# Kernel tuning notes

Hardware: AMD Instinct MI355X
Metric: run time of the kernel (lower is better)

The kernel has to match this reference:

```python
import jax, jax.numpy as jnp
import numpy as np

# PyTorch GRU cell math (gate order: r, z, n)

def _gru_cell(x, h, Wih_l, Whh_l, bih_l, bhh_l):
    # x: [B,F], h: [B,F]
    xg = x @ Wih_l.T + bih_l          # [B,3F]
    hg = h @ Whh_l.T + bhh_l          # [B,3F]
    xr, xz, xn = jnp.split(xg, 3, axis=-1)
    hr, hz, hn = jnp.split(hg, 3, axis=-1)
    r = jax.nn.sigmoid(xr + hr)
    z = jax.nn.sigmoid(xz + hz)
    n = jnp.tanh(xn + r * hn)
    return (1.0 - z) * n + z * h


def _gru_seq(x, Wih_l, Whh_l, bih_l, bhh_l):
    # x: [B,S,Fin] -> (outputs [B,S,F], last hidden [B,F]); zero initial state
    B, S, _ = x.shape
    F = Whh_l.shape[1]
    xg = jnp.einsum('bsi,gi->bsg', x, Wih_l) + bih_l  # [B,S,3F]
    def step(h, xg_t):
        hg = h @ Whh_l.T + bhh_l
        xr, xz, xn = jnp.split(xg_t, 3, axis=-1)
        hr, hz, hn = jnp.split(hg, 3, axis=-1)
        r = jax.nn.sigmoid(xr + hr)
        z = jax.nn.sigmoid(xz + hz)
        n = jnp.tanh(xn + r * hn)
        h_new = (1.0 - z) * n + z * h
        return h_new, h_new
    h0 = jnp.zeros((B, F), dtype=x.dtype)
    hT, ys = jax.lax.scan(step, h0, jnp.swapaxes(xg, 0, 1))
    return jnp.swapaxes(ys, 0, 1), hT


def setup_inputs() -> dict:
    key = jax.random.key(0)
    B, H, T = 32, 48, 16
    S_DIM, A_DIM, R_DIM, F, L = 64, 16, 8, 256, 2
    ks = jax.random.split(key, 20)
    k = 1.0 / np.sqrt(F)
    def xav(kk, shape):
        fan_in, fan_out = shape[1], shape[0]
        lim = np.sqrt(6.0 / (fan_in + fan_out))
        return jax.random.uniform(kk, shape, jnp.float32, -lim, lim)
    return {
        'history_s': jax.random.normal(ks[0], (B, H, S_DIM), jnp.float32),
        'history_a': jax.random.normal(ks[1], (B, H, A_DIM), jnp.float32),
        'present_s': jax.random.normal(ks[2], (B, S_DIM), jnp.float32),
        'future_a':  jax.random.normal(ks[3], (B, T, A_DIM), jnp.float32),
        'Ws':  xav(ks[4], (F, S_DIM)),
        'bs':  jnp.zeros((F,), jnp.float32),
        'Wa':  xav(ks[5], (F, A_DIM)),
        'ba':  jnp.zeros((F,), jnp.float32),
        'Wih': jax.random.uniform(ks[6], (L, 3 * F, F), jnp.float32, -k, k),
        'Whh': jax.random.uniform(ks[7], (L, 3 * F, F), jnp.float32, -k, k),
        'bih': jax.random.uniform(ks[8], (L, 3 * F), jnp.float32, -k, k),
        'bhh': jax.random.uniform(ks[9], (L, 3 * F), jnp.float32, -k, k),
        'Wr':  xav(ks[10], (R_DIM, F)),
        'br':  jnp.zeros((R_DIM,), jnp.float32),
        'Wso': xav(ks[11], (S_DIM, F)),
        'bso': jnp.zeros((S_DIM,), jnp.float32),
    }


def reference(history_s, history_a, present_s, future_a,
              Ws, bs, Wa, ba, Wih, Whh, bih, bhh, Wr, br, Wso, bso):
    # drop_rate = 0 -> DeterministicDropout is identity. Since the GRU is causal,
    # and the history prefix (history_s_a) is unchanged across rollout iterations,
    # re-running the GRU over the full growing history each step (the original
    # O(T^2) loop) is mathematically identical to carrying hidden state
    # incrementally. We implement the exact-equivalent O(T) form.
    L = Wih.shape[0]
    B = present_s.shape[0]
    F = Whh.shape[2]

    # embed history and run the stacked GRU over it once (zero init state)
    hist = jnp.einsum('bhs,fs->bhf', history_s, Ws) + bs \
         + jnp.einsum('bha,fa->bhf', history_a, Wa) + ba
    seq = jnp.tanh(hist)                                   # [B,H,F]
    hiddens = []
    for l in range(L):
        seq, hT = _gru_seq(seq, Wih[l], Whh[l], bih[l], bhh[l])
        hiddens.append(hT)
    hidden0 = jnp.stack(hiddens, axis=0)                   # [L,B,F]

    present_feat = present_s @ Ws.T + bs                   # [B,F]
    fa_feat = jnp.einsum('bta,fa->btf', future_a, Wa) + ba # [B,T,F]

    def rollout(carry, fa_t):
        pf, hidden = carry
        x = jnp.tanh(pf + fa_t)                            # [B,F]
        new_h = []
        inp = x
        for l in range(L):
            h_l = _gru_cell(inp, hidden[l], Wih[l], Whh[l], bih[l], bhh[l])
            new_h.append(h_l)
            inp = h_l
        hidden_new = jnp.stack(new_h, axis=0)
        r = jnp.tanh(inp @ Wr.T + br)                      # [B,R]
        s = jnp.tanh(inp @ Wso.T + bso)                    # [B,S]
        pf_new = s @ Ws.T + bs
        return (pf_new, hidden_new), (r, s)

    (_, _), (rs, ss) = jax.lax.scan(rollout, (present_feat, hidden0),
                                    jnp.swapaxes(fa_feat, 0, 1))
    future_r = jnp.swapaxes(rs, 0, 1)                      # [B,T,R]
    future_s = jnp.swapaxes(ss, 0, 1)                      # [B,T,S]
    return future_r, future_s
```

## Files before the change

### kernel.cpp

```cpp
#include <hip/hip_runtime.h>
#include <math.h>


#define BLK 256
#define CH  36
#define BST 292

#define O_XQ    0
#define O_HQ    1168
#define O_H1Q   2336
#define O_PART  3504
#define O_SST   6768
#define O_BI    7024
#define O_BH    7072
#define O_BSO   7120
#define O_BR    7184
#define O_WSOF  7200
#define O_WRF   23840
#define LDS_FLOATS 25920
#define LDS_BYTES  (LDS_FLOATS * 4)

#define O_SEQ  0
#define O_H0R  393216
#define O_H1R  917504
#define WS_FLOATS 1441792
#define POISON_BYTES (WS_FLOATS * 4)

using vf4 = __attribute__((ext_vector_type(4))) float;

__device__ __forceinline__ float dotv(vf4 a, vf4 b, float acc) {
  acc = fmaf(a[0], b[0], acc); acc = fmaf(a[1], b[1], acc);
  acc = fmaf(a[2], b[2], acc); acc = fmaf(a[3], b[3], acc);
  return acc;
}
__device__ __forceinline__ float hsum(vf4 v) { return (v[0]+v[1]) + (v[2]+v[3]); }

__device__ __forceinline__ bool valid4(vf4 v) {
  return fabsf(v[0]) < 1.0e30f && fabsf(v[1]) < 1.0e30f &&
         fabsf(v[2]) < 1.0e30f && fabsf(v[3]) < 1.0e30f;
}

__device__ __forceinline__ void llc_issue4(vf4& v, const float* p) {
  asm volatile("global_load_dwordx4 %0, %1, off sc0 sc1"
               : "=&v"(v) : "v"(p) : "memory");
}
__device__ __forceinline__ void llc_storef(float* p, float v) {
  asm volatile("global_store_dword %0, %1, off sc0 sc1" :: "v"(p), "v"(v) : "memory");
}
__device__ __forceinline__ void vwait() {
  asm volatile("s_waitcnt vmcnt(0)" ::: "memory");
  __builtin_amdgcn_sched_barrier(0);
}

extern "C" __global__ void __launch_bounds__(BLK, 1)
gru_rollout_kernel(const float* __restrict__ hist_s,
                   const float* __restrict__ hist_a,
                   const float* __restrict__ present_s,
                   const float* __restrict__ future_a,
                   const float* __restrict__ Ws, const float* __restrict__ bs,
                   const float* __restrict__ Wa, const float* __restrict__ ba,
                   const float* __restrict__ Wih, const float* __restrict__ Whh,
                   const float* __restrict__ bih, const float* __restrict__ bhh,
                   const float* __restrict__ Wr, const float* __restrict__ br,
                   const float* __restrict__ Wso, const float* __restrict__ bso,
                   float* __restrict__ out, float* __restrict__ wsf)
{
  extern __shared__ float lds[];
  float* XQ   = lds + O_XQ;
  float* HQ   = lds + O_HQ;
  float* H1Q  = lds + O_H1Q;
  float* PART = lds + O_PART;
  float* SST  = lds + O_SST;
  float* BI   = lds + O_BI;
  float* BH   = lds + O_BH;
  float* BSO  = lds + O_BSO;
  float* BR   = lds + O_BR;
  float* WSOF = lds + O_WSOF;
  float* WRF  = lds + O_WRF;

  const int tid = threadIdx.x;
  const int bid = blockIdx.x;
  const int gid = bid & 7;
  const int mem = bid >> 3;
  const bool isL0 = (mem < 16);
  const int fc = mem & 15;
  const int layer = isL0 ? 0 : 1;

  const int jp = tid >> 4;
  const int ks = tid & 15;

  float* seq = wsf + O_SEQ;
  float* h0r = wsf + O_H0R;
  float* h1r = wsf + O_H1R;

  const int sb = tid >> 6, srem = tid & 63;
  const int sko = srem >> 3, ssl = srem & 7;
  const int goff = sko * 32 + ssl * 4;
  const int loff = sb * BST + sko * CH + ssl * 4;
  const int gvec = (gid * 4 + sb) * 256 + goff;

  auto poll1 = [&](float* d, const float* p) {
    vf4 v; int g = 0;
    for (;;) {
      llc_issue4(v, p); vwait();
      if (valid4(v) || ++g > (1 << 18)) break;
    }
    *(vf4*)d = v;
  };
  auto poll2 = [&](float* d1, const float* p1, float* d2, const float* p2) {
    vf4 v1, v2; int g = 0;
    for (;;) {
      llc_issue4(v1, p1); llc_issue4(v2, p2); vwait();
      if ((valid4(v1) && valid4(v2)) || ++g > (1 << 18)) break;
    }
    *(vf4*)d1 = v1; *(vf4*)d2 = v2;
  };
  auto zeroH = [&](float* d) { *(vf4*)d = (vf4){0.f, 0.f, 0.f, 0.f}; };

  vf4 w[3][8];
  {
    const float* src = (ks < 8) ? Wih : Whh;
    const int cb = (ks & 7) * 32;
    #pragma unroll
    for (int r = 0; r < 3; ++r) {
      int j = jp * 3 + r;
      int grow = (layer * 768) + (j >> 4) * 256 + fc * 16 + (j & 15);
      const float* wr = src + grow * 256 + cb;
      #pragma unroll
      for (int c = 0; c < 8; ++c) w[r][c] = *(const vf4*)(wr + c * 4);
    }
  }
  const float* xq_base = (ks < 8) ? (XQ + ks * CH) : (HQ + (ks - 8) * CH);

  auto cell = [&](float* dst) {
    __syncthreads();
    float a0[4], a1[4], a2[4];
    #pragma unroll
    for (int b = 0; b < 4; ++b) { a0[b] = 0.f; a1[b] = 0.f; a2[b] = 0.f; }
    #pragma unroll
    for (int b = 0; b < 4; ++b) {
      const vf4* xb = (const vf4*)(xq_base + b * BST);
      vf4 x0 = xb[0], x1 = xb[1], x2 = xb[2], x3 = xb[3];
      vf4 x4 = xb[4], x5 = xb[5], x6 = xb[6], x7 = xb[7];
      float a = a0[b];
      a = dotv(w[0][0], x0, a); a = dotv(w[0][1], x1, a);
      a = dotv(w[0][2], x2, a); a = dotv(w[0][3], x3, a);
      a = dotv(w[0][4], x4, a); a = dotv(w[0][5], x5, a);
      a = dotv(w[0][6], x6, a); a = dotv(w[0][7], x7, a);
      a0[b] = a; a = a1[b];
      a = dotv(w[1][0], x0, a); a = dotv(w[1][1], x1, a);
      a = dotv(w[1][2], x2, a); a = dotv(w[1][3], x3, a);
      a = dotv(w[1][4], x4, a); a = dotv(w[1][5], x5, a);
      a = dotv(w[1][6], x6, a); a = dotv(w[1][7], x7, a);
      a1[b] = a; a = a2[b];
      a = dotv(w[2][0], x0, a); a = dotv(w[2][1], x1, a);
      a = dotv(w[2][2], x2, a); a = dotv(w[2][3], x3, a);
      a = dotv(w[2][4], x4, a); a = dotv(w[2][5], x5, a);
      a = dotv(w[2][6], x6, a); a = dotv(w[2][7], x7, a);
      a2[b] = a;
    }
    #pragma unroll
    for (int b = 0; b < 4; ++b) {
      PART[(jp * 3 + 0) * 68 + b * 16 + ks] = a0[b];
      PART[(jp * 3 + 1) * 68 + b * 16 + ks] = a1[b];
      PART[(jp * 3 + 2) * 68 + b * 16 + ks] = a2[b];
    }
    __syncthreads();
    if (tid < 64) {
      int i = tid >> 2, b = tid & 3;
      const vf4* pr4 = (const vf4*)(PART + i * 68 + b * 16);
      const vf4* pz4 = (const vf4*)(PART + (16 + i) * 68 + b * 16);
      const vf4* pn4 = (const vf4*)(PART + (32 + i) * 68 + b * 16);
      float pr = hsum(pr4[0]) + hsum(pr4[1]) + hsum(pr4[2]) + hsum(pr4[3])
               + BI[i] + BH[i];
      float pz = hsum(pz4[0]) + hsum(pz4[1]) + hsum(pz4[2]) + hsum(pz4[3])
               + BI[16 + i] + BH[16 + i];
      float xn = hsum(pn4[0]) + hsum(pn4[1]) + BI[32 + i];
      float hn = hsum(pn4[2]) + hsum(pn4[3]) + BH[32 + i];
      float rg = 1.f / (1.f + expf(-pr));
      float zg = 1.f / (1.f + expf(-pz));
      float ng = tanhf(xn + rg * hn);
      int f = fc * 16 + i;
      float hp = HQ[b * BST + (f >> 5) * CH + (f & 31)];
      llc_storef(dst + (gid * 4 + b) * 256 + f, (1.f - zg) * ng + zg * hp);
    }
  };

  auto heads = [&](int tt) {
    int so = tid >> 2, b = tid & 3;
    const vf4* wrow = (const vf4*)(WSOF + so * 260);
    float a = BSO[so];
    #pragma unroll
    for (int ko = 0; ko < 8; ++ko) {
      const vf4* hv = (const vf4*)(H1Q + b * BST + ko * CH);
      a = dotv(wrow[ko * 8 + 0], hv[0], a); a = dotv(wrow[ko * 8 + 1], hv[1], a);
      a = dotv(wrow[ko * 8 + 2], hv[2], a); a = dotv(wrow[ko * 8 + 3], hv[3], a);
      a = dotv(wrow[ko * 8 + 4], hv[4], a); a = dotv(wrow[ko * 8 + 5], hv[5], a);
      a = dotv(wrow[ko * 8 + 6], hv[6], a); a = dotv(wrow[ko * 8 + 7], hv[7], a);
    }
    float sv = tanhf(a);
    SST[b * 64 + so] = sv;
    if (mem == 0) {
      out[4096 + ((gid * 4 + b) * 16 + tt) * 64 + so] = sv;
      if (tid < 32) {
        int q = tid >> 2;
        const vf4* wr2 = (const vf4*)(WRF + q * 260);
        float ar = BR[q];
        #pragma unroll
        for (int ko = 0; ko < 8; ++ko) {
          const vf4* hv = (const vf4*)(H1Q + b * BST + ko * CH);
          #pragma unroll
          for (int c = 0; c < 8; ++c) ar = dotv(wr2[ko * 8 + c], hv[c], ar);
        }
        out[((gid * 4 + b) * 16 + tt) * 8 + q] = tanhf(ar);
      }
    }
  };

  auto xdot = [&](int t) {
    const int f = tid;
    float a0 = bs[f], a1 = a0, a2 = a0, a3 = a0;
    const vf4* wsr = (const vf4*)(Ws + f * 64);
    #pragma unroll 4
    for (int c = 0; c < 16; ++c) {
      vf4 wv = wsr[c];
      a0 = dotv(wv, *(const vf4*)(SST + 0 * 64 + c * 4), a0);
      a1 = dotv(wv, *(const vf4*)(SST + 1 * 64 + c * 4), a1);
      a2 = dotv(wv, *(const vf4*)(SST + 2 * 64 + c * 4), a2);
      a3 = dotv(wv, *(const vf4*)(SST + 3 * 64 + c * 4), a3);
    }
    const vf4* war = (const vf4*)(Wa + f * 16);
    vf4 w0 = war[0], w1 = war[1], w2 = war[2], w3 = war[3];
    float x4[4] = {a0, a1, a2, a3};
    #pragma unroll
    for (int b = 0; b < 4; ++b) {
      const vf4* fa = (const vf4*)(future_a + ((gid * 4 + b) * 16 + t) * 16);
      float a = ba[f] + x4[b];
      a = dotv(w0, fa[0], a); a = dotv(w1, fa[1], a);
      a = dotv(w2, fa[2], a); a = dotv(w3, fa[3], a);
      XQ[b * BST + (f >> 5) * CH + (f & 31)] = tanhf(a);
    }
  };

  if (tid < 48) {
    int g = tid >> 4, i = tid & 15;
    int grow = layer * 768 + g * 256 + fc * 16 + i;
    BI[tid] = bih[grow];
    BH[tid] = bhh[grow];
  }
  if (isL0) {
    for (int idx = tid; idx < 64 * 256; idx += BLK) {
      int r = idx >> 8, k = idx & 255;
      WSOF[r * 260 + k] = Wso[r * 256 + k];
    }
    for (int idx = tid; idx < 8 * 256; idx += BLK) {
      int r = idx >> 8, k = idx & 255;
      WRF[r * 260 + k] = Wr[r * 256 + k];
    }
    if (tid < 64) BSO[tid] = bso[tid];
    if (tid < 8)  BR[tid] = br[tid];
  }
  for (int e = mem * 1536 + tid; e < mem * 1536 + 1536; e += BLK) {
    int b = e / 12288, rem = e % 12288, t = rem >> 8, f = rem & 255;
    int gb = gid * 4 + b;
    const float* hs = hist_s + (gb * 48 + t) * 64;
    const float* ha = hist_a + (gb * 48 + t) * 16;
    const float* wsr = Ws + f * 64;
    const float* war = Wa + f * 16;
    float a = bs[f] + ba[f];
    for (int k = 0; k < 64; ++k) a = fmaf(wsr[k], hs[k], a);
    for (int k = 0; k < 16; ++k) a = fmaf(war[k], ha[k], a);
    llc_storef(&seq[(gb * 48 + t) * 256 + f], tanhf(a));
  }
  __syncthreads();

  for (int u = 0; u < 64; ++u) {
    if (isL0) {
      if (u < 48) {
        if (u == 0) {
          poll1(XQ + loff, seq + ((gid * 4 + sb) * 48 + u) * 256 + goff);
          zeroH(HQ + loff);
        } else {
          poll2(XQ + loff, seq + ((gid * 4 + sb) * 48 + u) * 256 + goff,
                HQ + loff, h0r + (u - 1) * 8192 + gvec);
        }
        cell(h0r + u * 8192);
      } else {
        const int t = u - 48;
        if (t == 0) {
          SST[tid] = present_s[(gid * 4 + (tid >> 6)) * 64 + (tid & 63)];
          poll1(HQ + loff, h0r + (u - 1) * 8192 + gvec);
          __syncthreads();
        } else {
          poll2(HQ + loff, h0r + (u - 1) * 8192 + gvec,
                H1Q + loff, h1r + (u - 1) * 8192 + gvec);
          __syncthreads();
          heads(t - 1);
          __syncthreads();
        }
        xdot(t);
        cell(h0r + u * 8192);
      }
    } else {
      if (u == 0) {
        poll1(XQ + loff, h0r + u * 8192 + gvec);
        zeroH(HQ + loff);
      } else {
        poll2(XQ + loff, h0r + u * 8192 + gvec,
              HQ + loff, h1r + (u - 1) * 8192 + gvec);
      }
      cell(h1r + u * 8192);
    }
  }

  if (isL0 && mem == 0) {
    poll1(H1Q + loff, h1r + 63 * 8192 + gvec);
    __syncthreads();
    heads(15);
  }
}

extern "C" void kernel_launch(void* const* d_in, const int* in_sizes, int n_in,
                              void* d_out, int out_size, void* d_ws, size_t ws_size,
                              hipStream_t stream) {
  (void)in_sizes; (void)n_in; (void)out_size; (void)ws_size;
  const float* hist_s    = (const float*)d_in[0];
  const float* hist_a    = (const float*)d_in[1];
  const float* present_s = (const float*)d_in[2];
  const float* future_a  = (const float*)d_in[3];
  const float* Ws  = (const float*)d_in[4];
  const float* bs  = (const float*)d_in[5];
  const float* Wa  = (const float*)d_in[6];
  const float* ba  = (const float*)d_in[7];
  const float* Wih = (const float*)d_in[8];
  const float* Whh = (const float*)d_in[9];
  const float* bih = (const float*)d_in[10];
  const float* bhh = (const float*)d_in[11];
  const float* Wr  = (const float*)d_in[12];
  const float* br  = (const float*)d_in[13];
  const float* Wso = (const float*)d_in[14];
  const float* bso = (const float*)d_in[15];
  float* out = (float*)d_out;
  float* wsf = (float*)d_ws;

  hipMemsetAsync(d_ws, 0x7F, POISON_BYTES, stream);
  hipFuncSetAttribute(reinterpret_cast<const void*>(gru_rollout_kernel),
                      hipFuncAttributeMaxDynamicSharedMemorySize, LDS_BYTES);
  hipLaunchKernelGGL(gru_rollout_kernel, dim3(256), dim3(BLK), LDS_BYTES, stream,
                     hist_s, hist_a, present_s, future_a,
                     Ws, bs, Wa, ba, Wih, Whh, bih, bhh, Wr, br, Wso, bso,
                     out, wsf);
}
```

Measured before the change: 344.8 us.

## Poll per-slice ready flags instead of poisoned data vectors between GRU steps

Each block now publishes a small per-step, per-layer ready flag after its hidden-state slice is written (wait on stores, then one flag store). Consumers spin on one or two flag words, with s_sleep between attempts, and then read the data in a single burst. Before, they repeatedly reloaded full data vectors and checked them for poison values. This is meant to cut LLC traffic and contention from many blocks spinning on wide loads. In exchange, every recurrent step gets an extra store-wait and an extra flag-then-data round trip on the critical path.

```diff
diff --git a/kernel.cpp b/kernel.cpp
--- a/kernel.cpp
+++ b/kernel.cpp
@@ -23,7 +23,8 @@
 #define O_SEQ  0
 #define O_H0R  393216
 #define O_H1R  917504
-#define WS_FLOATS 1441792
+#define O_CAN  1441792
+#define WS_FLOATS 1458176
 #define POISON_BYTES (WS_FLOATS * 4)
 
 using vf4 = __attribute__((ext_vector_type(4))) float;
@@ -43,6 +44,19 @@
 __device__ __forceinline__ void llc_issue4(vf4& v, const float* p) {
   asm volatile("global_load_dwordx4 %0, %1, off sc0 sc1"
                : "=&v"(v) : "v"(p) : "memory");
+}
+__device__ __forceinline__ float llc_loadf(const float* p) {
+  float v;
+  asm volatile("global_load_dword %0, %1, off sc0 sc1\n\ts_waitcnt vmcnt(0)"
+               : "=&v"(v) : "v"(p) : "memory");
+  return v;
+}
+__device__ __forceinline__ void llc_loadf2(float& a, float& b,
+                                           const float* p0, const float* p1) {
+  asm volatile("global_load_dword %0, %2, off sc0 sc1\n\t"
+               "global_load_dword %1, %3, off sc0 sc1\n\t"
+               "s_waitcnt vmcnt(0)"
+               : "=&v"(a), "=&v"(b) : "v"(p0), "v"(p1) : "memory");
 }
 __device__ __forceinline__ void llc_storef(float* p, float v) {
   asm volatile("global_store_dword %0, %1, off sc0 sc1" :: "v"(p), "v"(v) : "memory");
@@ -92,28 +106,53 @@
   float* seq = wsf + O_SEQ;
   float* h0r = wsf + O_H0R;
   float* h1r = wsf + O_H1R;
+  float* can = wsf + O_CAN;
 
   const int sb = tid >> 6, srem = tid & 63;
   const int sko = srem >> 3, ssl = srem & 7;
   const int goff = sko * 32 + ssl * 4;
   const int loff = sb * BST + sko * CH + ssl * 4;
   const int gvec = (gid * 4 + sb) * 256 + goff;
-
-  auto poll1 = [&](float* d, const float* p) {
+  const int slice = goff >> 4;
+
+  auto canp = [&](int u, int l) {
+    return can + ((u * 8 + gid) * 2 + l) * 16 + slice;
+  };
+  auto canp_mine = [&](int u) {
+    return can + ((u * 8 + gid) * 2 + layer) * 16 + fc;
+  };
+
+  auto cpoll1 = [&](const float* c) {
+    int g = 0;
+    while (llc_loadf(c) > 2.0f) {
+      __builtin_amdgcn_s_sleep(1);
+      if (++g > (1 << 18)) break;
+    }
+  };
+  auto cpoll2 = [&](const float* c0, const float* c1) {
+    int g = 0;
+    for (;;) {
+      float a, b;
+      llc_loadf2(a, b, c0, c1);
+      if ((a < 2.0f && b < 2.0f) || ++g > (1 << 18)) break;
+      __builtin_amdgcn_s_sleep(1);
+    }
+  };
+  auto burst1 = [&](float* d, const float* p) {
+    vf4 v; llc_issue4(v, p); vwait(); *(vf4*)d = v;
+  };
+  auto burst2 = [&](float* d1, const float* p1, float* d2, const float* p2) {
+    vf4 v1, v2; llc_issue4(v1, p1); llc_issue4(v2, p2); vwait();
+    *(vf4*)d1 = v1; *(vf4*)d2 = v2;
+  };
+  auto dpoll1 = [&](float* d, const float* p) {
     vf4 v; int g = 0;
     for (;;) {
       llc_issue4(v, p); vwait();
       if (valid4(v) || ++g > (1 << 18)) break;
+      __builtin_amdgcn_s_sleep(1);
     }
     *(vf4*)d = v;
-  };
-  auto poll2 = [&](float* d1, const float* p1, float* d2, const float* p2) {
-    vf4 v1, v2; int g = 0;
-    for (;;) {
-      llc_issue4(v1, p1); llc_issue4(v2, p2); vwait();
-      if ((valid4(v1) && valid4(v2)) || ++g > (1 << 18)) break;
-    }
-    *(vf4*)d1 = v1; *(vf4*)d2 = v2;
   };
   auto zeroH = [&](float* d) { *(vf4*)d = (vf4){0.f, 0.f, 0.f, 0.f}; };
 
@@ -132,7 +171,7 @@
   }
   const float* xq_base = (ks < 8) ? (XQ + ks * CH) : (HQ + (ks - 8) * CH);
 
-  auto cell = [&](float* dst) {
+  auto cell = [&](float* dst, float* cp) {
     __syncthreads();
     float a0[4], a1[4], a2[4];
     #pragma unroll
@@ -183,6 +222,8 @@
       int f = fc * 16 + i;
       float hp = HQ[b * BST + (f >> 5) * CH + (f & 31)];
       llc_storef(dst + (gid * 4 + b) * 256 + f, (1.f - zg) * ng + zg * hp);
+      asm volatile("s_waitcnt vmcnt(0)" ::: "memory");
+      if (tid == 0) llc_storef(cp, 1.0f);
     }
   };
 
@@ -277,44 +318,60 @@
   for (int u = 0; u < 64; ++u) {
     if (isL0) {
       if (u < 48) {
+        const float* seqp = seq + ((gid * 4 + sb) * 48 + u) * 256 + goff;
         if (u == 0) {
-          poll1(XQ + loff, seq + ((gid * 4 + sb) * 48 + u) * 256 + goff);
+          dpoll1(XQ + loff, seqp);
           zeroH(HQ + loff);
         } else {
-          poll2(XQ + loff, seq + ((gid * 4 + sb) * 48 + u) * 256 + goff,
-                HQ + loff, h0r + (u - 1) * 8192 + gvec);
+          cpoll1(canp(u - 1, 0));
+          vf4 vx, vh;
+          llc_issue4(vx, seqp);
+          llc_issue4(vh, h0r + (u - 1) * 8192 + gvec);
+          vwait();
+          int g = 0;
+          while (!valid4(vx) && ++g < (1 << 18)) {
+            __builtin_amdgcn_s_sleep(1);
+            llc_issue4(vx, seqp); vwait();
+          }
+          *(vf4*)(XQ + loff) = vx;
+          *(vf4*)(HQ + loff) = vh;
         }
-        cell(h0r + u * 8192);
+        cell(h0r + u * 8192, canp_mine(u));
       } else {
         const int t = u - 48;
         if (t == 0) {
           SST[tid] = present_s[(gid * 4 + (tid >> 6)) * 64 + (tid & 63)];
-          poll1(HQ + loff, h0r + (u - 1) * 8192 + gvec);
+          cpoll1(canp(u - 1, 0));
+          burst1(HQ + loff, h0r + (u - 1) * 8192 + gvec);
           __syncthreads();
         } else {
-          poll2(HQ + loff, h0r + (u - 1) * 8192 + gvec,
-                H1Q + loff, h1r + (u - 1) * 8192 + gvec);
+          cpoll2(canp(u - 1, 0), canp(u - 1, 1));
+          burst2(HQ + loff,  h0r + (u - 1) * 8192 + gvec,
+                 H1Q + loff, h1r + (u - 1) * 8192 + gvec);
           __syncthreads();
           heads(t - 1);
           __syncthreads();
         }
         xdot(t);
-        cell(h0r + u * 8192);
+        cell(h0r + u * 8192, canp_mine(u));
       }
     } else {
       if (u == 0) {
-        poll1(XQ + loff, h0r + u * 8192 + gvec);
+        cpoll1(canp(0, 0));
+        burst1(XQ + loff, h0r + gvec);
         zeroH(HQ + loff);
       } else {
-        poll2(XQ + loff, h0r + u * 8192 + gvec,
-              HQ + loff, h1r + (u - 1) * 8192 + gvec);
+        cpoll2(canp(u, 0), canp(u - 1, 1));
+        burst2(XQ + loff, h0r + u * 8192 + gvec,
+               HQ + loff, h1r + (u - 1) * 8192 + gvec);
       }
-      cell(h1r + u * 8192);
+      cell(h1r + u * 8192, canp_mine(u));
     }
   }
 
   if (isL0 && mem == 0) {
-    poll1(H1Q + loff, h1r + 63 * 8192 + gvec);
+    cpoll1(canp(63, 1));
+    burst1(H1Q + loff, h1r + 63 * 8192 + gvec);
     __syncthreads();
     heads(15);
   }
```

New measurement: 433.9 us. +25.8%, slower.

## Repartition GRU blocks to one batch row per group with wider feature slices

Applied to the files above, without the earlier changes.

Blocks now map one batch element per group (32 groups) and 64 output features per block (4 blocks per layer), instead of 4 batch rows per group and 16 features per block. Each thread holds a full 128-wide slice of three weight rows in registers, and only the first wavefront polls for the cross-block data each step. Polling loops also back off with s_sleep after a few misses. Head weights are stored transposed in LDS and the head matvecs are computed for a single batch row. The aim is to cut the PART reduction and per-block LDS traffic and to shorten the inter-block dependency chain. The cost is much higher register pressure (96 vf4 weights per thread) and possible spills or lower occupancy.

```diff
diff --git a/kernel.cpp b/kernel.cpp
--- a/kernel.cpp
+++ b/kernel.cpp
@@ -3,21 +3,19 @@
 
 
 #define BLK 256
-#define CH  36
-#define BST 292
 
 #define O_XQ    0
-#define O_HQ    1168
-#define O_H1Q   2336
-#define O_PART  3504
-#define O_SST   6768
-#define O_BI    7024
-#define O_BH    7072
-#define O_BSO   7120
-#define O_BR    7184
-#define O_WSOF  7200
-#define O_WRF   23840
-#define LDS_FLOATS 25920
+#define O_HQ    264
+#define O_H1Q   528
+#define O_PART  792
+#define O_SST   2328
+#define O_BI    2392
+#define O_BH    2584
+#define O_BSO   2776
+#define O_BR    2840
+#define O_WST   2848
+#define O_WRF   19488
+#define LDS_FLOATS 21568
 #define LDS_BYTES  (LDS_FLOATS * 4)
 
 #define O_SEQ  0
@@ -33,7 +31,6 @@
   acc = fmaf(a[2], b[2], acc); acc = fmaf(a[3], b[3], acc);
   return acc;
 }
-__device__ __forceinline__ float hsum(vf4 v) { return (v[0]+v[1]) + (v[2]+v[3]); }
 
 __device__ __forceinline__ bool valid4(vf4 v) {
   return fabsf(v[0]) < 1.0e30f && fabsf(v[1]) < 1.0e30f &&
@@ -75,183 +72,151 @@
   float* BH   = lds + O_BH;
   float* BSO  = lds + O_BSO;
   float* BR   = lds + O_BR;
-  float* WSOF = lds + O_WSOF;
+  float* WST  = lds + O_WST;
   float* WRF  = lds + O_WRF;
 
   const int tid = threadIdx.x;
   const int bid = blockIdx.x;
-  const int gid = bid & 7;
-  const int mem = bid >> 3;
-  const bool isL0 = (mem < 16);
-  const int fc = mem & 15;
+  const int gid = bid & 31;
+  const int mem = bid >> 5;
+  const bool isL0 = (mem < 4);
+  const int fc = mem & 3;
   const int layer = isL0 ? 0 : 1;
 
-  const int jp = tid >> 4;
-  const int ks = tid & 15;
+  const int jp = tid >> 2;
+  const int ks = tid & 3;
 
   float* seq = wsf + O_SEQ;
   float* h0r = wsf + O_H0R;
   float* h1r = wsf + O_H1R;
 
-  const int sb = tid >> 6, srem = tid & 63;
-  const int sko = srem >> 3, ssl = srem & 7;
-  const int goff = sko * 32 + ssl * 4;
-  const int loff = sb * BST + sko * CH + ssl * 4;
-  const int gvec = (gid * 4 + sb) * 256 + goff;
-
-  auto poll1 = [&](float* d, const float* p) {
+  const int lane = tid;
+  const int goff = lane * 4;
+  const int loff = (lane >> 5) * 132 + (lane & 31) * 4;
+  const int gvec = gid * 256 + goff;
+
+  auto pollA = [&](float* d, const float* p) {
     vf4 v; int g = 0;
     for (;;) {
       llc_issue4(v, p); vwait();
-      if (valid4(v) || ++g > (1 << 18)) break;
+      if (valid4(v)) break;
+      if (++g > 32) __builtin_amdgcn_s_sleep(1);
+      if (g > (1 << 18)) break;
     }
     *(vf4*)d = v;
   };
-  auto poll2 = [&](float* d1, const float* p1, float* d2, const float* p2) {
+  auto pollB = [&](float* d1, const float* p1, float* d2, const float* p2) {
     vf4 v1, v2; int g = 0;
     for (;;) {
       llc_issue4(v1, p1); llc_issue4(v2, p2); vwait();
-      if ((valid4(v1) && valid4(v2)) || ++g > (1 << 18)) break;
+      if (valid4(v1) && valid4(v2)) break;
+      if (++g > 32) __builtin_amdgcn_s_sleep(1);
+      if (g > (1 << 18)) break;
     }
     *(vf4*)d1 = v1; *(vf4*)d2 = v2;
   };
   auto zeroH = [&](float* d) { *(vf4*)d = (vf4){0.f, 0.f, 0.f, 0.f}; };
 
-  vf4 w[3][8];
+  vf4 w[3][32];
   {
-    const float* src = (ks < 8) ? Wih : Whh;
-    const int cb = (ks & 7) * 32;
+    const float* src = (ks < 2) ? Wih : Whh;
+    const int cb = (ks & 1) * 128;
     #pragma unroll
     for (int r = 0; r < 3; ++r) {
-      int j = jp * 3 + r;
-      int grow = (layer * 768) + (j >> 4) * 256 + fc * 16 + (j & 15);
+      int grow = layer * 768 + r * 256 + fc * 64 + jp;
       const float* wr = src + grow * 256 + cb;
       #pragma unroll
-      for (int c = 0; c < 8; ++c) w[r][c] = *(const vf4*)(wr + c * 4);
-    }
-  }
-  const float* xq_base = (ks < 8) ? (XQ + ks * CH) : (HQ + (ks - 8) * CH);
+      for (int c = 0; c < 32; ++c) w[r][c] = *(const vf4*)(wr + c * 4);
+    }
+  }
+  const float* xb = (ks < 2) ? (XQ + ks * 132) : (HQ + (ks - 2) * 132);
 
   auto cell = [&](float* dst) {
     __syncthreads();
-    float a0[4], a1[4], a2[4];
+    float a0 = 0.f, a1 = 0.f, a2 = 0.f;
+    const vf4* xp = (const vf4*)xb;
     #pragma unroll
-    for (int b = 0; b < 4; ++b) { a0[b] = 0.f; a1[b] = 0.f; a2[b] = 0.f; }
-    #pragma unroll
-    for (int b = 0; b < 4; ++b) {
-      const vf4* xb = (const vf4*)(xq_base + b * BST);
-      vf4 x0 = xb[0], x1 = xb[1], x2 = xb[2], x3 = xb[3];
-      vf4 x4 = xb[4], x5 = xb[5], x6 = xb[6], x7 = xb[7];
-      float a = a0[b];
-      a = dotv(w[0][0], x0, a); a = dotv(w[0][1], x1, a);
-      a = dotv(w[0][2], x2, a); a = dotv(w[0][3], x3, a);
-      a = dotv(w[0][4], x4, a); a = dotv(w[0][5], x5, a);
-      a = dotv(w[0][6], x6, a); a = dotv(w[0][7], x7, a);
-      a0[b] = a; a = a1[b];
-      a = dotv(w[1][0], x0, a); a = dotv(w[1][1], x1, a);
-      a = dotv(w[1][2], x2, a); a = dotv(w[1][3], x3, a);
-      a = dotv(w[1][4], x4, a); a = dotv(w[1][5], x5, a);
-      a = dotv(w[1][6], x6, a); a = dotv(w[1][7], x7, a);
-      a1[b] = a; a = a2[b];
-      a = dotv(w[2][0], x0, a); a = dotv(w[2][1], x1, a);
-      a = dotv(w[2][2], x2, a); a = dotv(w[2][3], x3, a);
-      a = dotv(w[2][4], x4, a); a = dotv(w[2][5], x5, a);
-      a = dotv(w[2][6], x6, a); a = dotv(w[2][7], x7, a);
-      a2[b] = a;
-    }
-    #pragma unroll
-    for (int b = 0; b < 4; ++b) {
-      PART[(jp * 3 + 0) * 68 + b * 16 + ks] = a0[b];
-      PART[(jp * 3 + 1) * 68 + b * 16 + ks] = a1[b];
-      PART[(jp * 3 + 2) * 68 + b * 16 + ks] = a2[b];
-    }
+    for (int c4 = 0; c4 < 8; ++c4) {
+      vf4 x0 = xp[c4 * 4 + 0], x1 = xp[c4 * 4 + 1];
+      vf4 x2 = xp[c4 * 4 + 2], x3 = xp[c4 * 4 + 3];
+      a0 = dotv(w[0][c4 * 4 + 0], x0, a0); a0 = dotv(w[0][c4 * 4 + 1], x1, a0);
+      a0 = dotv(w[0][c4 * 4 + 2], x2, a0); a0 = dotv(w[0][c4 * 4 + 3], x3, a0);
+      a1 = dotv(w[1][c4 * 4 + 0], x0, a1); a1 = dotv(w[1][c4 * 4 + 1], x1, a1);
+      a1 = dotv(w[1][c4 * 4 + 2], x2, a1); a1 = dotv(w[1][c4 * 4 + 3], x3, a1);
+      a2 = dotv(w[2][c4 * 4 + 0], x0, a2); a2 = dotv(w[2][c4 * 4 + 1], x1, a2);
+      a2 = dotv(w[2][c4 * 4 + 2], x2, a2); a2 = dotv(w[2][c4 * 4 + 3], x3, a2);
+    }
+    PART[jp * 8 + ks] = a0;
+    PART[(64 + jp) * 8 + ks] = a1;
+    PART[(128 + jp) * 8 + ks] = a2;
     __syncthreads();
     if (tid < 64) {
-      int i = tid >> 2, b = tid & 3;
-      const vf4* pr4 = (const vf4*)(PART + i * 68 + b * 16);
-      const vf4* pz4 = (const vf4*)(PART + (16 + i) * 68 + b * 16);
-      const vf4* pn4 = (const vf4*)(PART + (32 + i) * 68 + b * 16);
-      float pr = hsum(pr4[0]) + hsum(pr4[1]) + hsum(pr4[2]) + hsum(pr4[3])
-               + BI[i] + BH[i];
-      float pz = hsum(pz4[0]) + hsum(pz4[1]) + hsum(pz4[2]) + hsum(pz4[3])
-               + BI[16 + i] + BH[16 + i];
-      float xn = hsum(pn4[0]) + hsum(pn4[1]) + BI[32 + i];
-      float hn = hsum(pn4[2]) + hsum(pn4[3]) + BH[32 + i];
+      int i = tid;
+      vf4 p0 = *(const vf4*)(PART + i * 8);
+      vf4 p1 = *(const vf4*)(PART + (64 + i) * 8);
+      vf4 p2 = *(const vf4*)(PART + (128 + i) * 8);
+      float pr = (p0[0] + p0[1]) + (p0[2] + p0[3]) + BI[i] + BH[i];
+      float pz = (p1[0] + p1[1]) + (p1[2] + p1[3]) + BI[64 + i] + BH[64 + i];
+      float xn = p2[0] + p2[1] + BI[128 + i];
+      float hn = p2[2] + p2[3] + BH[128 + i];
       float rg = 1.f / (1.f + expf(-pr));
       float zg = 1.f / (1.f + expf(-pz));
       float ng = tanhf(xn + rg * hn);
-      int f = fc * 16 + i;
-      float hp = HQ[b * BST + (f >> 5) * CH + (f & 31)];
-      llc_storef(dst + (gid * 4 + b) * 256 + f, (1.f - zg) * ng + zg * hp);
+      int f = fc * 64 + i;
+      float hp = HQ[(f >> 7) * 132 + (f & 127)];
+      llc_storef(dst + gid * 256 + f, (1.f - zg) * ng + zg * hp);
     }
   };
 
   auto heads = [&](int tt) {
-    int so = tid >> 2, b = tid & 3;
-    const vf4* wrow = (const vf4*)(WSOF + so * 260);
-    float a = BSO[so];
-    #pragma unroll
-    for (int ko = 0; ko < 8; ++ko) {
-      const vf4* hv = (const vf4*)(H1Q + b * BST + ko * CH);
-      a = dotv(wrow[ko * 8 + 0], hv[0], a); a = dotv(wrow[ko * 8 + 1], hv[1], a);
-      a = dotv(wrow[ko * 8 + 2], hv[2], a); a = dotv(wrow[ko * 8 + 3], hv[3], a);
-      a = dotv(wrow[ko * 8 + 4], hv[4], a); a = dotv(wrow[ko * 8 + 5], hv[5], a);
-      a = dotv(wrow[ko * 8 + 6], hv[6], a); a = dotv(wrow[ko * 8 + 7], hv[7], a);
-    }
-    float sv = tanhf(a);
-    SST[b * 64 + so] = sv;
-    if (mem == 0) {
-      out[4096 + ((gid * 4 + b) * 16 + tt) * 64 + so] = sv;
-      if (tid < 32) {
-        int q = tid >> 2;
-        const vf4* wr2 = (const vf4*)(WRF + q * 260);
-        float ar = BR[q];
-        #pragma unroll
-        for (int ko = 0; ko < 8; ++ko) {
-          const vf4* hv = (const vf4*)(H1Q + b * BST + ko * CH);
-          #pragma unroll
-          for (int c = 0; c < 8; ++c) ar = dotv(wr2[ko * 8 + c], hv[c], ar);
-        }
-        out[((gid * 4 + b) * 16 + tt) * 8 + q] = tanhf(ar);
-      }
+    if (tid < 64) {
+      int so = tid;
+      float a = BSO[so];
+      #pragma unroll 16
+      for (int k = 0; k < 256; ++k)
+        a = fmaf(WST[k * 65 + so], H1Q[(k >> 7) * 132 + (k & 127)], a);
+      float sv = tanhf(a);
+      SST[so] = sv;
+      if (mem == 0) out[4096 + (gid * 16 + tt) * 64 + so] = sv;
+    }
+    if (mem == 0 && tid >= 64 && tid < 72) {
+      int q = tid - 64;
+      const vf4* wrow = (const vf4*)(WRF + q * 260);
+      const vf4* h0c = (const vf4*)(H1Q);
+      const vf4* h1c = (const vf4*)(H1Q + 132);
+      float a = BR[q];
+      #pragma unroll
+      for (int c = 0; c < 32; ++c) a = dotv(wrow[c], h0c[c], a);
+      #pragma unroll
+      for (int c = 0; c < 32; ++c) a = dotv(wrow[32 + c], h1c[c], a);
+      out[(gid * 16 + tt) * 8 + q] = tanhf(a);
     }
   };
 
   auto xdot = [&](int t) {
     const int f = tid;
-    float a0 = bs[f], a1 = a0, a2 = a0, a3 = a0;
     const vf4* wsr = (const vf4*)(Ws + f * 64);
-    #pragma unroll 4
-    for (int c = 0; c < 16; ++c) {
-      vf4 wv = wsr[c];
-      a0 = dotv(wv, *(const vf4*)(SST + 0 * 64 + c * 4), a0);
-      a1 = dotv(wv, *(const vf4*)(SST + 1 * 64 + c * 4), a1);
-      a2 = dotv(wv, *(const vf4*)(SST + 2 * 64 + c * 4), a2);
-      a3 = dotv(wv, *(const vf4*)(SST + 3 * 64 + c * 4), a3);
-    }
+    float a = bs[f] + ba[f];
+    #pragma unroll
+    for (int c = 0; c < 16; ++c)
+      a = dotv(wsr[c], *(const vf4*)(SST + c * 4), a);
     const vf4* war = (const vf4*)(Wa + f * 16);
-    vf4 w0 = war[0], w1 = war[1], w2 = war[2], w3 = war[3];
-    float x4[4] = {a0, a1, a2, a3};
-    #pragma unroll
-    for (int b = 0; b < 4; ++b) {
-      const vf4* fa = (const vf4*)(future_a + ((gid * 4 + b) * 16 + t) * 16);
-      float a = ba[f] + x4[b];
-      a = dotv(w0, fa[0], a); a = dotv(w1, fa[1], a);
-      a = dotv(w2, fa[2], a); a = dotv(w3, fa[3], a);
-      XQ[b * BST + (f >> 5) * CH + (f & 31)] = tanhf(a);
-    }
-  };
-
-  if (tid < 48) {
-    int g = tid >> 4, i = tid & 15;
-    int grow = layer * 768 + g * 256 + fc * 16 + i;
+    const vf4* fa = (const vf4*)(future_a + (gid * 16 + t) * 16);
+    a = dotv(war[0], fa[0], a); a = dotv(war[1], fa[1], a);
+    a = dotv(war[2], fa[2], a); a = dotv(war[3], fa[3], a);
+    XQ[(f >> 7) * 132 + (f & 127)] = tanhf(a);
+  };
+
+  if (tid < 192) {
+    int r = tid >> 6, i = tid & 63;
+    int grow = layer * 768 + r * 256 + fc * 64 + i;
     BI[tid] = bih[grow];
     BH[tid] = bhh[grow];
   }
   if (isL0) {
     for (int idx = tid; idx < 64 * 256; idx += BLK) {
-      int r = idx >> 8, k = idx & 255;
-      WSOF[r * 260 + k] = Wso[r * 256 + k];
+      int so = idx >> 8, k = idx & 255;
+      WST[k * 65 + so] = Wso[so * 256 + k];
     }
     for (int idx = tid; idx < 8 * 256; idx += BLK) {
       int r = idx >> 8, k = idx & 255;
@@ -261,39 +226,43 @@
     if (tid < 8)  BR[tid] = br[tid];
   }
   for (int e = mem * 1536 + tid; e < mem * 1536 + 1536; e += BLK) {
-    int b = e / 12288, rem = e % 12288, t = rem >> 8, f = rem & 255;
-    int gb = gid * 4 + b;
-    const float* hs = hist_s + (gb * 48 + t) * 64;
-    const float* ha = hist_a + (gb * 48 + t) * 16;
+    int t = e >> 8, f = e & 255;
+    const float* hs = hist_s + (gid * 48 + t) * 64;
+    const float* ha = hist_a + (gid * 48 + t) * 16;
     const float* wsr = Ws + f * 64;
     const float* war = Wa + f * 16;
     float a = bs[f] + ba[f];
     for (int k = 0; k < 64; ++k) a = fmaf(wsr[k], hs[k], a);
     for (int k = 0; k < 16; ++k) a = fmaf(war[k], ha[k], a);
-    llc_storef(&seq[(gb * 48 + t) * 256 + f], tanhf(a));
+    llc_storef(&seq[(gid * 48 + t) * 256 + f], tanhf(a));
   }
   __syncthreads();
 
   for (int u = 0; u < 64; ++u) {
     if (isL0) {
       if (u < 48) {
-        if (u == 0) {
-          poll1(XQ + loff, seq + ((gid * 4 + sb) * 48 + u) * 256 + goff);
-          zeroH(HQ + loff);
-        } else {
-          poll2(XQ + loff, seq + ((gid * 4 + sb) * 48 + u) * 256 + goff,
-                HQ + loff, h0r + (u - 1) * 8192 + gvec);
+        if (tid < 64) {
+          if (u == 0) {
+            pollA(XQ + loff, seq + (gid * 48) * 256 + goff);
+            zeroH(HQ + loff);
+          } else {
+            pollB(XQ + loff, seq + (gid * 48 + u) * 256 + goff,
+                  HQ + loff, h0r + (u - 1) * 8192 + gvec);
+          }
         }
         cell(h0r + u * 8192);
       } else {
         const int t = u - 48;
         if (t == 0) {
-          SST[tid] = present_s[(gid * 4 + (tid >> 6)) * 64 + (tid & 63)];
-          poll1(HQ + loff, h0r + (u - 1) * 8192 + gvec);
+          if (tid < 64) {
+            SST[tid] = present_s[gid * 64 + tid];
+            pollA(HQ + loff, h0r + 47 * 8192 + gvec);
+          }
           __syncthreads();
         } else {
-          poll2(HQ + loff, h0r + (u - 1) * 8192 + gvec,
-                H1Q + loff, h1r + (u - 1) * 8192 + gvec);
+          if (tid < 64)
+            pollB(HQ + loff,  h0r + (u - 1) * 8192 + gvec,
+                  H1Q + loff, h1r + (u - 1) * 8192 + gvec);
           __syncthreads();
           heads(t - 1);
           __syncthreads();
@@ -302,19 +271,21 @@
         cell(h0r + u * 8192);
       }
     } else {
-      if (u == 0) {
-        poll1(XQ + loff, h0r + u * 8192 + gvec);
-        zeroH(HQ + loff);
-      } else {
-        poll2(XQ + loff, h0r + u * 8192 + gvec,
-              HQ + loff, h1r + (u - 1) * 8192 + gvec);
+      if (tid < 64) {
+        if (u == 0) {
+          pollA(XQ + loff, h0r + gvec);
+          zeroH(HQ + loff);
+        } else {
+          pollB(XQ + loff, h0r + u * 8192 + gvec,
+                HQ + loff, h1r + (u - 1) * 8192 + gvec);
+        }
       }
       cell(h1r + u * 8192);
     }
   }
 
   if (isL0 && mem == 0) {
-    poll1(H1Q + loff, h1r + 63 * 8192 + gvec);
+    if (tid < 64) pollA(H1Q + loff, h1r + 63 * 8192 + gvec);
     __syncthreads();
     heads(15);
   }
```

New measurement: 441.2 us. 28.0% more time.
